# Optimization experiments

Measured on AMD Instinct MI355X. Metric: run time of the kernel, lower is better.

The kernel has to match this reference:

```python
import jax, jax.numpy as jnp
import numpy as np

D_STATE = 16

def setup_inputs() -> dict:
    key = jax.random.key(0)
    ks = jax.random.split(key, 7)
    B, L, d_model = 2, 4096, 1024
    d_inner, d_conv, d_state = 2048, 4, D_STATE
    s = 0.02
    return {
        "x": jax.random.normal(ks[0], (B, L, d_model), jnp.float32),
        "W_in": jax.random.normal(ks[1], (2 * d_inner, d_model), jnp.float32) * s,
        "conv_w": jax.random.normal(ks[2], (d_inner, d_conv), jnp.float32) * 0.3,
        "conv_b": jax.random.normal(ks[3], (d_inner,), jnp.float32) * 0.1,
        "W_xproj": jax.random.normal(ks[4], (2 * d_state + d_inner, d_inner), jnp.float32) * s,
        "D": jnp.ones((d_inner,), jnp.float32),
        "W_out": jax.random.normal(ks[5], (d_model, d_inner), jnp.float32) * s,
    }

def _silu(v):
    return v * jax.nn.sigmoid(v)

def reference(x, W_in, conv_w, conv_b, W_xproj, D, W_out):
    Bsz, L, _ = x.shape
    d_inner, d_conv = conv_w.shape
    d_state = D_STATE
    # in_proj -> split into x branch and gate z
    xz = jnp.einsum('bld,ed->ble', x, W_in)           # [B,L,2*d_inner]
    xb, z = xz[..., :d_inner], xz[..., d_inner:]
    # causal depthwise conv1d (left pad d_conv-1, truncate to L)
    xpad = jnp.pad(xb, ((0, 0), (d_conv - 1, 0), (0, 0)))
    xc = conv_b
    for k in range(d_conv):  # tiny fixed kernel loop
        xc = xc + conv_w[:, k] * xpad[:, k:k + L, :]
    xc = _silu(xc)                                    # [B,L,d_inner]
    # x_proj -> B, C, delta
    proj = jnp.einsum('bld,ed->ble', xc, W_xproj)     # [B,L,2*d_state+d_inner]
    Bm = proj[..., :d_state]
    Cm = proj[..., d_state:2 * d_state]
    delta = jax.nn.softplus(proj[..., 2 * d_state:])  # [B,L,d_inner]
    # selective 'scan' as written collapses: y[b,l,d] = delta*x * sum_s B*C + D*x
    bc = jnp.einsum('bls,bls->bl', Bm, Cm)            # [B,L]
    y = delta * xc * bc[..., None] + D * xc
    y = y * _silu(z)
    return jnp.einsum('bld,ed->ble', y, W_out)        # [B,L,d_model]
```

## Files before the change

### kernel.cpp

```cpp
#include <hip/hip_runtime.h>
#include <hip/hip_bf16.h>
#include <cstdint>
#include <cmath>

typedef __bf16 bf16x8 __attribute__((ext_vector_type(8)));
typedef float  f32x4  __attribute__((ext_vector_type(4)));
typedef unsigned short u16x8 __attribute__((ext_vector_type(8)));

#define BT 128
#define BK 64

__device__ __forceinline__ float bf2f(unsigned short h) {
  union { unsigned int u; float f; } v; v.u = ((unsigned int)h) << 16;
  return v.f;
}
__device__ __forceinline__ unsigned short f2bf(float x) {
  union { float f; unsigned int u; } v; v.f = x;
  unsigned int r = v.u + 0x7fffu + ((v.u >> 16) & 1u);
  return (unsigned short)(r >> 16);
}

__device__ __forceinline__ void gld_lds16(const void* g, void* l) {
  __builtin_amdgcn_global_load_lds(
      (const __attribute__((address_space(1))) unsigned int*)g,
      (__attribute__((address_space(3))) unsigned int*)l,
      16, 0, 0);
}

__device__ __forceinline__ void cvt4(const float* __restrict__ in,
                                     unsigned short* __restrict__ out, int i) {
  float4 v = reinterpret_cast<const float4*>(in)[i];
  ushort4 o;
  o.x = f2bf(v.x); o.y = f2bf(v.y); o.z = f2bf(v.z); o.w = f2bf(v.w);
  reinterpret_cast<ushort4*>(out)[i] = o;
}

__global__ void cvt_head(const float* __restrict__ x, unsigned short* __restrict__ xb,
                         const float* __restrict__ W_in, unsigned short* __restrict__ wb) {
  int b = blockIdx.x;
  if (b < 8192) cvt4(x, xb, b * 256 + threadIdx.x);
  else          cvt4(W_in, wb, (b - 8192) * 256 + threadIdx.x);
}

__device__ void conv_strip8(const unsigned short* __restrict__ xz,
                            const float* __restrict__ conv_w,
                            const float* __restrict__ conv_b,
                            unsigned short* __restrict__ xc,
                            int strip, int tid) {
  const int bl0  = strip * 8;
  const int seq0 = bl0 & ~4095;
  const int c0   = tid * 8;
  float w[4][8], bb[8];
#pragma unroll
  for (int j = 0; j < 8; ++j) {
    float4 wr = reinterpret_cast<const float4*>(conv_w)[c0 + j];
    w[0][j] = wr.x; w[1][j] = wr.y; w[2][j] = wr.z; w[3][j] = wr.w;
    bb[j] = conv_b[c0 + j];
  }
  u16x8 rowv[8];
  float win[3][8];
#pragma unroll
  for (int i = 0; i < 3; ++i) {
    int r = bl0 - 3 + i;
    if (r >= seq0) {
      u16x8 v = *reinterpret_cast<const u16x8*>(xz + (size_t)r * 4096 + c0);
#pragma unroll
      for (int j = 0; j < 8; ++j) win[i][j] = bf2f(v[j]);
    } else {
#pragma unroll
      for (int j = 0; j < 8; ++j) win[i][j] = 0.f;
    }
  }
#pragma unroll
  for (int i = 0; i < 8; ++i)
    rowv[i] = *reinterpret_cast<const u16x8*>(xz + (size_t)(bl0 + i) * 4096 + c0);

#pragma unroll
  for (int i = 0; i < 8; ++i) {
    u16x8 o;
#pragma unroll
    for (int j = 0; j < 8; ++j) {
      float cur = bf2f(rowv[i][j]);
      float a = bb[j] + w[0][j] * win[0][j] + w[1][j] * win[1][j]
                      + w[2][j] * win[2][j] + w[3][j] * cur;
      o[j] = f2bf(a * __builtin_amdgcn_rcpf(1.f + __expf(-a)));
      win[0][j] = win[1][j]; win[1][j] = win[2][j]; win[2][j] = cur;
    }
    *reinterpret_cast<u16x8*>(xc + (size_t)(bl0 + i) * 2048 + c0) = o;
  }
}

__global__ void mid_fused(const unsigned short* __restrict__ xz,
                          const float* __restrict__ conv_w,
                          const float* __restrict__ conv_b,
                          unsigned short* __restrict__ xc,
                          const float* __restrict__ W_xproj, unsigned short* __restrict__ wx_bf,
                          const float* __restrict__ W_out,   unsigned short* __restrict__ wo_bf) {
  int b = blockIdx.x;
  if (b < 1024) { conv_strip8(xz, conv_w, conv_b, xc, b, threadIdx.x); return; }
  b -= 1024;
  if (b < 4160) { cvt4(W_xproj, wx_bf, b * 256 + threadIdx.x); return; }
  cvt4(W_out, wo_bf, (b - 4160) * 256 + threadIdx.x);
}

template <int GUARD_N, int OUT_F32>
__global__ __launch_bounds__(256, 2)
void gemm_bt(const unsigned short* __restrict__ A,
             const unsigned short* __restrict__ B,
             void* __restrict__ Cv,
             int N, int K, int ldA, int ldB, int ldC)
{
  __shared__ __align__(16) unsigned short sA[BT * BK];
  __shared__ __align__(16) unsigned short sB[BT * BK];

  const int tid  = threadIdx.x;
  const int lane = tid & 63;
  const int wave = tid >> 6;
  const int row0 = blockIdx.x * BT;
  const int col0 = blockIdx.y * BT;

  const int wrow = (wave & 1) * 64;
  const int wcol = (wave >> 1) * 64;
  const int l15  = lane & 15;
  const int q    = lane >> 4;

  f32x4 acc[4][4];
#pragma unroll
  for (int i = 0; i < 4; ++i)
#pragma unroll
    for (int j = 0; j < 4; ++j)
      acc[i][j] = (f32x4){0.f, 0.f, 0.f, 0.f};

  const int nk = K / BK;
  for (int kt = 0; kt < nk; ++kt) {
    const int k0 = kt * BK;
#pragma unroll
    for (int t = 0; t < 4; ++t) {
      int c  = t * 256 + tid;
      int r  = c >> 3;
      int g  = c & 7;
      int gs = (g ^ (r & 7)) * 8;
      gld_lds16(A + (size_t)(row0 + r) * ldA + k0 + gs, (void*)(sA + c * 8));
      int br = col0 + r;
      if (GUARD_N) br = (br < N) ? br : (N - 1);
      gld_lds16(B + (size_t)br * ldB + k0 + gs, (void*)(sB + c * 8));
    }
    __syncthreads();

#pragma unroll
    for (int kk = 0; kk < BK; kk += 32) {
      const int grb = kk >> 3;
      bf16x8 af[4], bfr[4];
#pragma unroll
      for (int i = 0; i < 4; ++i) {
        int ar = wrow + i * 16 + l15;
        af[i] = *reinterpret_cast<const bf16x8*>(
            sA + ar * BK + (((grb + q) ^ (ar & 7)) << 3));
        int br = wcol + i * 16 + l15;
        bfr[i] = *reinterpret_cast<const bf16x8*>(
            sB + br * BK + (((grb + q) ^ (br & 7)) << 3));
      }
#pragma unroll
      for (int i = 0; i < 4; ++i)
#pragma unroll
        for (int j = 0; j < 4; ++j)
          acc[i][j] = __builtin_amdgcn_mfma_f32_16x16x32_bf16(af[i], bfr[j], acc[i][j], 0, 0, 0);
    }
    __syncthreads();
  }

#pragma unroll
  for (int i = 0; i < 4; ++i) {
#pragma unroll
    for (int j = 0; j < 4; ++j) {
      int colw = col0 + wcol + j * 16 + l15;
      if (GUARD_N && colw >= N) continue;
#pragma unroll
      for (int r = 0; r < 4; ++r) {
        int roww = row0 + wrow + i * 16 + q * 4 + r;
        if (OUT_F32)
          ((float*)Cv)[(size_t)roww * ldC + colw] = acc[i][j][r];
        else
          ((unsigned short*)Cv)[(size_t)roww * ldC + colw] = f2bf(acc[i][j][r]);
      }
    }
  }
}

#define BARX() do { __builtin_amdgcn_sched_barrier(0); \
                    __builtin_amdgcn_s_barrier(); \
                    __builtin_amdgcn_sched_barrier(0); } while (0)
#define VMW(n) asm volatile("s_waitcnt vmcnt(" #n ")" ::: "memory")
#define LGKM0() asm volatile("s_waitcnt lgkmcnt(0)" ::: "memory")

#define STAGE_A(b, h, kt) do { \
  const unsigned short* _p = Ab + (size_t)((h) * 128) * ldA + (kt) * 64; \
  gld_lds16(_p,                     (void*)&sA[b][((h) * 128      + rr) * 64 + (g8 << 3)]); \
  gld_lds16(_p + (size_t)64 * ldA,  (void*)&sA[b][((h) * 128 + 64 + rr) * 64 + (g8 << 3)]); \
} while (0)

#define STAGE_B(b, h, kt) do { \
  const unsigned short* _p = Bb + (size_t)((h) * 128) * ldB + (kt) * 64; \
  gld_lds16(_p,                     (void*)&sB[b][((h) * 128      + rr) * 64 + (g8 << 3)]); \
  gld_lds16(_p + (size_t)64 * ldB,  (void*)&sB[b][((h) * 128 + 64 + rr) * 64 + (g8 << 3)]); \
} while (0)

#define RD_A_SET(dst, b, p) do { \
  dst[0][0] = *reinterpret_cast<const bf16x8*>(&sA[b][aOff + (2*(p)    ) * 1024 + kph0]); \
  dst[0][1] = *reinterpret_cast<const bf16x8*>(&sA[b][aOff + (2*(p)    ) * 1024 + kph1]); \
  dst[1][0] = *reinterpret_cast<const bf16x8*>(&sA[b][aOff + (2*(p) + 1) * 1024 + kph0]); \
  dst[1][1] = *reinterpret_cast<const bf16x8*>(&sA[b][aOff + (2*(p) + 1) * 1024 + kph1]); \
} while (0)

#define RD_B_SET(dst, b) do { \
  dst[0][0] = *reinterpret_cast<const bf16x8*>(&sB[b][bOff + 0 * 1024 + kph0]); \
  dst[0][1] = *reinterpret_cast<const bf16x8*>(&sB[b][bOff + 0 * 1024 + kph1]); \
  dst[1][0] = *reinterpret_cast<const bf16x8*>(&sB[b][bOff + 1 * 1024 + kph0]); \
  dst[1][1] = *reinterpret_cast<const bf16x8*>(&sB[b][bOff + 1 * 1024 + kph1]); \
  dst[2][0] = *reinterpret_cast<const bf16x8*>(&sB[b][bOff + 2 * 1024 + kph0]); \
  dst[2][1] = *reinterpret_cast<const bf16x8*>(&sB[b][bOff + 2 * 1024 + kph1]); \
  dst[3][0] = *reinterpret_cast<const bf16x8*>(&sB[b][bOff + 3 * 1024 + kph0]); \
  dst[3][1] = *reinterpret_cast<const bf16x8*>(&sB[b][bOff + 3 * 1024 + kph1]); \
} while (0)

#define MMA(i, j, k, Af, Bf) \
  acc[i][j] = __builtin_amdgcn_mfma_f32_16x16x32_bf16(Af[(i) & 1][k], Bf[j][k], acc[i][j], 0, 0, 0)

#define MFMA_PH(p, Af, Bf) do { \
  __builtin_amdgcn_s_setprio(1); \
  MMA(2*(p),   0, 0, Af, Bf); MMA(2*(p),   1, 0, Af, Bf); \
  MMA(2*(p),   2, 0, Af, Bf); MMA(2*(p),   3, 0, Af, Bf); \
  MMA(2*(p)+1, 0, 0, Af, Bf); MMA(2*(p)+1, 1, 0, Af, Bf); \
  MMA(2*(p)+1, 2, 0, Af, Bf); MMA(2*(p)+1, 3, 0, Af, Bf); \
  MMA(2*(p),   0, 1, Af, Bf); MMA(2*(p),   1, 1, Af, Bf); \
  MMA(2*(p),   2, 1, Af, Bf); MMA(2*(p),   3, 1, Af, Bf); \
  MMA(2*(p)+1, 0, 1, Af, Bf); MMA(2*(p)+1, 1, 1, Af, Bf); \
  MMA(2*(p)+1, 2, 1, Af, Bf); MMA(2*(p)+1, 3, 1, Af, Bf); \
  __builtin_amdgcn_s_setprio(0); \
} while (0)

template <int EPI>
__global__ __launch_bounds__(512, 2)
void gemm256(const unsigned short* __restrict__ A,
             const unsigned short* __restrict__ B,
             unsigned short* __restrict__ C,
             int K, int ldA, int ldB, int ldC, int ccsh,
             const unsigned short* __restrict__ XZ,
             const float* __restrict__ Dw,
             const float* __restrict__ BC)
{
  __shared__ __align__(16) unsigned short smem[4 * 256 * 64];
  unsigned short (*sA)[256 * 64] = (unsigned short (*)[256 * 64])smem;
  unsigned short (*sB)[256 * 64] = (unsigned short (*)[256 * 64])(smem + 2 * 256 * 64);

  const int tid  = threadIdx.x;
  const int lane = tid & 63;
  const int wave = tid >> 6;
  const int wm = wave >> 2;
  const int wn = wave & 3;
  const int l15 = lane & 15;
  const int q   = lane >> 4;

  const int nwg = gridDim.x;
  const int wg  = blockIdx.x;
  const int x   = wg & 7;
  const int c   = wg >> 3;
  const int CC  = 1 << ccsh;
  const int R   = (nwg >> 3) >> ccsh;
  const int row0 = ((x >> 1) * R + (c >> ccsh)) * 256;
  const int col0 = ((x & 1) * CC + (c & (CC - 1))) * 256;

  const int rr  = tid >> 3;
  const int g8  = tid & 7;
  const int gsw = ((g8 ^ (rr & 7)) << 3);
  const unsigned short* Ab = A + (size_t)(row0 + rr) * ldA + gsw;
  const unsigned short* Bb = B + (size_t)(col0 + rr) * ldB + gsw;

  const int aOff = (wm * 128 + l15) * 64;
  const int bOff = (wn * 64  + l15) * 64;
  const int a7   = l15 & 7;
  const int kph0 = ((q       ^ a7) << 3);
  const int kph1 = (((4 + q) ^ a7) << 3);

  f32x4 acc[8][4];
#pragma unroll
  for (int i = 0; i < 8; ++i)
#pragma unroll
    for (int j = 0; j < 4; ++j)
      acc[i][j] = (f32x4){0.f, 0.f, 0.f, 0.f};

  bf16x8 afe[2][2], afo[2][2];
  bf16x8 bfe[4][2], bfo[4][2];

  const int nk = K >> 6;
  STAGE_A(0, 0, 0); STAGE_A(0, 1, 0);
  STAGE_B(0, 0, 0); STAGE_B(0, 1, 0);
  STAGE_B(1, 0, 1); STAGE_B(1, 1, 1);
  VMW(4);
  BARX();
  RD_B_SET(bfe, 0); RD_A_SET(afe, 0, 0);

  const int niter = K >> 7;
  for (int it = 0; it < niter; ++it) {
    const int kt1 = 2 * it + 1;
    int ktE = 2 * it + 2; if (ktE > nk - 1) ktE = nk - 1;
    int ktO = 2 * it + 3; if (ktO > nk - 1) ktO = nk - 1;

    STAGE_A(1, 0, kt1);
    BARX();
    MFMA_PH(0, afe, bfe); RD_A_SET(afo, 0, 1);
    BARX();
    STAGE_A(1, 1, kt1);
    BARX();
    MFMA_PH(1, afo, bfe); RD_A_SET(afe, 0, 2);
    BARX();
    STAGE_B(0, 0, ktE);
    BARX();
    MFMA_PH(2, afe, bfe); RD_A_SET(afo, 0, 3);
    BARX();
    STAGE_B(0, 1, ktE);
    VMW(4);
    BARX();
    MFMA_PH(3, afo, bfe); RD_B_SET(bfo, 1); RD_A_SET(afe, 1, 0);
    BARX();

    STAGE_A(0, 0, ktE);
    BARX();
    MFMA_PH(0, afe, bfo); RD_A_SET(afo, 1, 1);
    BARX();
    STAGE_A(0, 1, ktE);
    BARX();
    MFMA_PH(1, afo, bfo); RD_A_SET(afe, 1, 2);
    BARX();
    STAGE_B(1, 0, ktO);
    BARX();
    MFMA_PH(2, afe, bfo); RD_A_SET(afo, 1, 3);
    BARX();
    STAGE_B(1, 1, ktO);
    VMW(4);
    BARX();
    MFMA_PH(3, afo, bfo); RD_B_SET(bfe, 0); RD_A_SET(afe, 0, 0);
    BARX();
  }

  VMW(0);
  LGKM0();
  BARX();
  {
    unsigned short* cs = smem;
#pragma unroll
    for (int i = 0; i < 8; ++i) {
      const int row = wm * 128 + i * 16 + q * 4;
#pragma unroll
      for (int j = 0; j < 4; ++j) {
        const int col = (wn * 64 + j * 16 + l15) ^ (q << 4);
#pragma unroll
        for (int r = 0; r < 4; ++r)
          cs[(row + r) * 256 + col] = f2bf(acc[i][j][r]);
      }
    }

    const int colf   = (tid * 8) & 255;
    const int rowofs = tid >> 5;
    const int colX   = col0 + colf;

    if (EPI == 0) {
      LGKM0();
      BARX();
#pragma unroll
      for (int s = 0; s < 16; ++s) {
        const int row  = s * 16 + rowofs;
        const int rcol = colf ^ (((row >> 2) & 3) << 4);
        u16x8 v = *reinterpret_cast<const u16x8*>(&cs[row * 256 + rcol]);
        *reinterpret_cast<u16x8*>(C + (size_t)(row0 + row) * ldC + colX) = v;
      }
    } else {
      float dj[8];
      float4 d0 = reinterpret_cast<const float4*>(Dw)[colX >> 2];
      float4 d1 = reinterpret_cast<const float4*>(Dw)[(colX >> 2) + 1];
      dj[0] = d0.x; dj[1] = d0.y; dj[2] = d0.z; dj[3] = d0.w;
      dj[4] = d1.x; dj[5] = d1.y; dj[6] = d1.z; dj[7] = d1.w;
      const size_t g0 = (size_t)(row0 + rowofs);
      u16x8 xc_c = *reinterpret_cast<const u16x8*>(A + g0 * ldA + colX);
      u16x8 zv_c = *reinterpret_cast<const u16x8*>(XZ + g0 * 4096 + 2048 + colX);
      float bc_c = BC[g0];

      LGKM0();
      BARX();

#pragma unroll
      for (int s = 0; s < 16; ++s) {
        u16x8 xc_n, zv_n; float bc_n;
        if (s < 15) {
          const size_t gn = (size_t)(row0 + (s + 1) * 16 + rowofs);
          xc_n = *reinterpret_cast<const u16x8*>(A + gn * ldA + colX);
          zv_n = *reinterpret_cast<const u16x8*>(XZ + gn * 4096 + 2048 + colX);
          bc_n = BC[gn];
        }
        const int row  = s * 16 + rowofs;
        const int rcol = colf ^ (((row >> 2) & 3) << 4);
        const size_t gr = (size_t)(row0 + row);
        u16x8 pv = *reinterpret_cast<const u16x8*>(&cs[row * 256 + rcol]);
        u16x8 o;
#pragma unroll
        for (int j = 0; j < 8; ++j) {
          float p  = bf2f(pv[j]);
          float delta = (p > 15.f) ? p : __logf(1.f + __expf(p));
          float xv = bf2f(xc_c[j]);
          float zz = bf2f(zv_c[j]);
          float y  = delta * xv * bc_c + dj[j] * xv;
          y *= zz * __builtin_amdgcn_rcpf(1.f + __expf(-zz));
          o[j] = f2bf(y);
        }
        *reinterpret_cast<u16x8*>(C + gr * ldC + colX) = o;
        if (s < 15) { xc_c = xc_n; zv_c = zv_n; bc_c = bc_n; }
      }
    }
  }
}

__global__ __launch_bounds__(256)
void proj_strip(const unsigned short* __restrict__ xc,
                const unsigned short* __restrict__ wx,
                float* __restrict__ bc)
{
  __shared__ float red[4][16 * 33];
  const int tid  = threadIdx.x;
  const int lane = tid & 63;
  const int wave = tid >> 6;
  const int l15  = lane & 15;
  const int q    = lane >> 4;
  const int row0 = blockIdx.x * 16;

  f32x4 acc[2];
  acc[0] = (f32x4){0.f, 0.f, 0.f, 0.f};
  acc[1] = (f32x4){0.f, 0.f, 0.f, 0.f};

  const int kbase = wave * 512;
#pragma unroll 4
  for (int kk = 0; kk < 512; kk += 32) {
    const int k = kbase + kk + q * 8;
    bf16x8 a0 = *reinterpret_cast<const bf16x8*>(&xc[(size_t)(row0 + l15) * 2048 + k]);
    bf16x8 b0 = *reinterpret_cast<const bf16x8*>(&wx[(size_t)(l15) * 2048 + k]);
    bf16x8 b1 = *reinterpret_cast<const bf16x8*>(&wx[(size_t)(16 + l15) * 2048 + k]);
    acc[0] = __builtin_amdgcn_mfma_f32_16x16x32_bf16(a0, b0, acc[0], 0, 0, 0);
    acc[1] = __builtin_amdgcn_mfma_f32_16x16x32_bf16(a0, b1, acc[1], 0, 0, 0);
  }

#pragma unroll
  for (int j = 0; j < 2; ++j)
#pragma unroll
    for (int r = 0; r < 4; ++r)
      red[wave][(q * 4 + r) * 33 + j * 16 + l15] = acc[j][r];
  __syncthreads();

  if (tid < 16) {
    float s = 0.f;
#pragma unroll
    for (int cc = 0; cc < 16; ++cc) {
      const int ib = tid * 33 + cc;
      float b  = red[0][ib] + red[1][ib] + red[2][ib] + red[3][ib];
      float cv = red[0][ib + 16] + red[1][ib + 16] + red[2][ib + 16] + red[3][ib + 16];
      s += b * cv;
    }
    bc[row0 + tid] = s;
  }
}

extern "C" void kernel_launch(void* const* d_in, const int* in_sizes, int n_in,
                              void* d_out, int out_size, void* d_ws, size_t ws_size,
                              hipStream_t stream) {
  const float* x       = (const float*)d_in[0];
  const float* W_in    = (const float*)d_in[1];
  const float* conv_w  = (const float*)d_in[2];
  const float* conv_b  = (const float*)d_in[3];
  const float* W_xproj = (const float*)d_in[4];
  const float* Dw      = (const float*)d_in[5];
  const float* W_out   = (const float*)d_in[6];
  float* out = (float*)d_out;

  unsigned short* xz_bf   = (unsigned short*)d_ws;
  unsigned short* xc_bf   = xz_bf  + (size_t)8192 * 4096;
  unsigned short* y_bf    = xc_bf  + (size_t)8192 * 2048;
  float*          bc_ws   = (float*)(y_bf + (size_t)8192 * 2048);
  unsigned short* xb_bf   = y_bf + (size_t)8192 * 2080;
  unsigned short* w_bf    = xb_bf  + (size_t)8192 * 1024;

  cvt_head<<<8192 + 4096, 256, 0, stream>>>(x, xb_bf, W_in, w_bf);
  gemm256<0><<<512, 512, 0, stream>>>(xb_bf, w_bf, xz_bf, 1024, 1024, 1024, 4096, 3,
                                      nullptr, nullptr, nullptr);
  mid_fused<<<1024 + 4160 + 2048, 256, 0, stream>>>(xz_bf, conv_w, conv_b, xc_bf,
                                                    W_xproj, xb_bf, W_out, w_bf);
  proj_strip<<<512, 256, 0, stream>>>(xc_bf, xb_bf, bc_ws);
  gemm256<1><<<256, 512, 0, stream>>>(xc_bf, xb_bf + (size_t)32 * 2048, y_bf,
                                      2048, 2048, 2048, 2048, 2,
                                      xz_bf, Dw, bc_ws);
  gemm_bt<0, 1><<<dim3(64, 8), 256, 0, stream>>>(y_bf, w_bf, out, 1024, 2048, 2048, 2048, 1024);
}
```

Before: 329.1 us.

## Fuse causal depthwise conv+SiLU into in_proj GEMM epilogue using LDS tile

The in_proj GEMM gets a new epilogue mode that computes the causal depthwise conv and SiLU for the x-branch columns directly from the output tile held in LDS. It writes xc alongside xz, so the separate conv pass no longer has to re-read xz from global memory. Only the first 3 rows of each 256-row tile need halo rows from the previous tile, and a small patch kernel with 32 blocks fills those rows afterwards. The cost is extra epilogue work and register pressure in the GEMM.

Measured after the change: 333.0 us. Within noise of the previous version (+1.2%).

```diff
diff --git a/kernel.cpp b/kernel.cpp
--- a/kernel.cpp
+++ b/kernel.cpp
@@ -42,51 +42,46 @@
   else          cvt4(W_in, wb, (b - 8192) * 256 + threadIdx.x);
 }
 
-__device__ void conv_strip8(const unsigned short* __restrict__ xz,
+__device__ void conv_patch3(const unsigned short* __restrict__ xz,
                             const float* __restrict__ conv_w,
                             const float* __restrict__ conv_b,
                             unsigned short* __restrict__ xc,
-                            int strip, int tid) {
-  const int bl0  = strip * 8;
-  const int seq0 = bl0 & ~4095;
+                            int stripe, int tid) {
+  const int row0 = stripe * 256;
+  const int seq0 = row0 & ~4095;
   const int c0   = tid * 8;
-  float w[4][8], bb[8];
+  float w0[8], w1[8], w2[8], w3[8], bb[8];
 #pragma unroll
   for (int j = 0; j < 8; ++j) {
     float4 wr = reinterpret_cast<const float4*>(conv_w)[c0 + j];
-    w[0][j] = wr.x; w[1][j] = wr.y; w[2][j] = wr.z; w[3][j] = wr.w;
+    w0[j] = wr.x; w1[j] = wr.y; w2[j] = wr.z; w3[j] = wr.w;
     bb[j] = conv_b[c0 + j];
   }
-  u16x8 rowv[8];
-  float win[3][8];
 #pragma unroll
   for (int i = 0; i < 3; ++i) {
-    int r = bl0 - 3 + i;
-    if (r >= seq0) {
-      u16x8 v = *reinterpret_cast<const u16x8*>(xz + (size_t)r * 4096 + c0);
-#pragma unroll
-      for (int j = 0; j < 8; ++j) win[i][j] = bf2f(v[j]);
-    } else {
-#pragma unroll
-      for (int j = 0; j < 8; ++j) win[i][j] = 0.f;
-    }
-  }
-#pragma unroll
-  for (int i = 0; i < 8; ++i)
-    rowv[i] = *reinterpret_cast<const u16x8*>(xz + (size_t)(bl0 + i) * 4096 + c0);
-
-#pragma unroll
-  for (int i = 0; i < 8; ++i) {
+    const int r = row0 + i;
+    u16x8 xr = *reinterpret_cast<const u16x8*>(xz + (size_t)r * 4096 + c0);
+    float h[3][8];
+#pragma unroll
+    for (int t = 0; t < 3; ++t) {
+      int rh = r - 3 + t;
+      if (rh >= seq0) {
+        u16x8 v = *reinterpret_cast<const u16x8*>(xz + (size_t)rh * 4096 + c0);
+#pragma unroll
+        for (int j = 0; j < 8; ++j) h[t][j] = bf2f(v[j]);
+      } else {
+#pragma unroll
+        for (int j = 0; j < 8; ++j) h[t][j] = 0.f;
+      }
+    }
     u16x8 o;
 #pragma unroll
     for (int j = 0; j < 8; ++j) {
-      float cur = bf2f(rowv[i][j]);
-      float a = bb[j] + w[0][j] * win[0][j] + w[1][j] * win[1][j]
-                      + w[2][j] * win[2][j] + w[3][j] * cur;
+      float a = bb[j] + w0[j] * h[0][j] + w1[j] * h[1][j]
+                      + w2[j] * h[2][j] + w3[j] * bf2f(xr[j]);
       o[j] = f2bf(a * __builtin_amdgcn_rcpf(1.f + __expf(-a)));
-      win[0][j] = win[1][j]; win[1][j] = win[2][j]; win[2][j] = cur;
-    }
-    *reinterpret_cast<u16x8*>(xc + (size_t)(bl0 + i) * 2048 + c0) = o;
+    }
+    *reinterpret_cast<u16x8*>(xc + (size_t)r * 2048 + c0) = o;
   }
 }
 
@@ -97,8 +92,8 @@
                           const float* __restrict__ W_xproj, unsigned short* __restrict__ wx_bf,
                           const float* __restrict__ W_out,   unsigned short* __restrict__ wo_bf) {
   int b = blockIdx.x;
-  if (b < 1024) { conv_strip8(xz, conv_w, conv_b, xc, b, threadIdx.x); return; }
-  b -= 1024;
+  if (b < 32) { conv_patch3(xz, conv_w, conv_b, xc, b, threadIdx.x); return; }
+  b -= 32;
   if (b < 4160) { cvt4(W_xproj, wx_bf, b * 256 + threadIdx.x); return; }
   cvt4(W_out, wo_bf, (b - 4160) * 256 + threadIdx.x);
 }
@@ -247,7 +242,10 @@
              int K, int ldA, int ldB, int ldC, int ccsh,
              const unsigned short* __restrict__ XZ,
              const float* __restrict__ Dw,
-             const float* __restrict__ BC)
+             const float* __restrict__ BC,
+             const float* __restrict__ CW,
+             const float* __restrict__ CB,
+             unsigned short* __restrict__ XC)
 {
   __shared__ __align__(16) unsigned short smem[4 * 256 * 64];
   unsigned short (*sA)[256 * 64] = (unsigned short (*)[256 * 64])smem;
@@ -374,7 +372,7 @@
         u16x8 v = *reinterpret_cast<const u16x8*>(&cs[row * 256 + rcol]);
         *reinterpret_cast<u16x8*>(C + (size_t)(row0 + row) * ldC + colX) = v;
       }
-    } else {
+    } else if (EPI == 1) {
       float dj[8];
       float4 d0 = reinterpret_cast<const float4*>(Dw)[colX >> 2];
       float4 d1 = reinterpret_cast<const float4*>(Dw)[(colX >> 2) + 1];
@@ -415,6 +413,45 @@
         *reinterpret_cast<u16x8*>(C + gr * ldC + colX) = o;
         if (s < 15) { xc_c = xc_n; zv_c = zv_n; bc_c = bc_n; }
       }
+    } else {
+      const bool doConv = (col0 < 2048);
+      float w0[8], w1[8], w2[8], w3[8], bb[8];
+      if (doConv) {
+#pragma unroll
+        for (int j = 0; j < 8; ++j) {
+          float4 wr = reinterpret_cast<const float4*>(CW)[colX + j];
+          w0[j] = wr.x; w1[j] = wr.y; w2[j] = wr.z; w3[j] = wr.w;
+        }
+        float4 b0 = reinterpret_cast<const float4*>(CB)[colX >> 2];
+        float4 b1 = reinterpret_cast<const float4*>(CB)[(colX >> 2) + 1];
+        bb[0] = b0.x; bb[1] = b0.y; bb[2] = b0.z; bb[3] = b0.w;
+        bb[4] = b1.x; bb[5] = b1.y; bb[6] = b1.z; bb[7] = b1.w;
+      }
+      LGKM0();
+      BARX();
+#pragma unroll
+      for (int s = 0; s < 16; ++s) {
+        const int row  = s * 16 + rowofs;
+        const int rcol = colf ^ (((row >> 2) & 3) << 4);
+        u16x8 v = *reinterpret_cast<const u16x8*>(&cs[row * 256 + rcol]);
+        *reinterpret_cast<u16x8*>(C + (size_t)(row0 + row) * ldC + colX) = v;
+        if (doConv && row >= 3) {
+          const int rc1 = colf ^ ((((row - 1) >> 2) & 3) << 4);
+          const int rc2 = colf ^ ((((row - 2) >> 2) & 3) << 4);
+          const int rc3 = colf ^ ((((row - 3) >> 2) & 3) << 4);
+          u16x8 x1 = *reinterpret_cast<const u16x8*>(&cs[(row - 1) * 256 + rc1]);
+          u16x8 x2 = *reinterpret_cast<const u16x8*>(&cs[(row - 2) * 256 + rc2]);
+          u16x8 x3 = *reinterpret_cast<const u16x8*>(&cs[(row - 3) * 256 + rc3]);
+          u16x8 o;
+#pragma unroll
+          for (int j = 0; j < 8; ++j) {
+            float a = bb[j] + w0[j] * bf2f(x3[j]) + w1[j] * bf2f(x2[j])
+                            + w2[j] * bf2f(x1[j]) + w3[j] * bf2f(v[j]);
+            o[j] = f2bf(a * __builtin_amdgcn_rcpf(1.f + __expf(-a)));
+          }
+          *reinterpret_cast<u16x8*>(XC + (size_t)(row0 + row) * 2048 + colX) = o;
+        }
+      }
     }
   }
 }
@@ -487,13 +524,15 @@
   unsigned short* w_bf    = xb_bf  + (size_t)8192 * 1024;
 
   cvt_head<<<8192 + 4096, 256, 0, stream>>>(x, xb_bf, W_in, w_bf);
-  gemm256<0><<<512, 512, 0, stream>>>(xb_bf, w_bf, xz_bf, 1024, 1024, 1024, 4096, 3,
-                                      nullptr, nullptr, nullptr);
-  mid_fused<<<1024 + 4160 + 2048, 256, 0, stream>>>(xz_bf, conv_w, conv_b, xc_bf,
-                                                    W_xproj, xb_bf, W_out, w_bf);
+  gemm256<2><<<512, 512, 0, stream>>>(xb_bf, w_bf, xz_bf, 1024, 1024, 1024, 4096, 3,
+                                      nullptr, nullptr, nullptr,
+                                      conv_w, conv_b, xc_bf);
+  mid_fused<<<32 + 4160 + 2048, 256, 0, stream>>>(xz_bf, conv_w, conv_b, xc_bf,
+                                                  W_xproj, xb_bf, W_out, w_bf);
   proj_strip<<<512, 256, 0, stream>>>(xc_bf, xb_bf, bc_ws);
   gemm256<1><<<256, 512, 0, stream>>>(xc_bf, xb_bf + (size_t)32 * 2048, y_bf,
                                       2048, 2048, 2048, 2048, 2,
-                                      xz_bf, Dw, bc_ws);
+                                      xz_bf, Dw, bc_ws,
+                                      nullptr, nullptr, nullptr);
   gemm_bt<0, 1><<<dim3(64, 8), 256, 0, stream>>>(y_bf, w_bf, out, 1024, 2048, 2048, 2048, 1024);
 }
```
